# Optimization experiments

Measured on AMD Instinct MI355X. Metric: run time of the kernel, lower is better.

## Reference

```python
import jax, jax.numpy as jnp
import numpy as np

B, LN, LT, D, DIN, H = 8, 64, 256, 1024, 2048, 4
LN_EPS = 1e-5
F16_EPS = float(np.finfo(np.float16).eps)


def setup_inputs() -> dict:
    key = jax.random.key(0)
    ks = jax.random.split(key, 16)
    n = lambda k, sh: jax.random.normal(k, sh, dtype=jnp.float32)
    s = 0.02
    z = lambda sh: jnp.zeros(sh, jnp.float32)
    return {
        "text_embeds": n(ks[0], (B, LT, D)),
        "node_embeds": n(ks[1], (B, LN, D)),
        "Wq": n(ks[2], (D, H * D)) * s, "bq": z((H * D,)),
        "Wk": n(ks[3], (D, H * D)) * s, "bk": z((H * D,)),
        "Wv": n(ks[4], (D, H * D)) * s, "bv": z((H * D,)),
        "Wo": n(ks[5], (H * D, D)) * s, "bo": z((D,)),
        "ln_g": jnp.ones((D,), jnp.float32), "ln_b": z((D,)),
        "aqW": n(ks[6], (D, D)) * s, "aqb": z((D,)),
        "akW": n(ks[7], (D, D)) * s, "akb": z((D,)),
        "att_v": n(ks[8], (D,)) * (1.0 / np.sqrt(D)),
        "att_b": z((D,)),
        "dp1W": n(ks[9], (D, DIN // 2)) * s, "dp1b": z((DIN // 2,)),
        "dp2W": n(ks[10], (DIN // 2, DIN)) * s, "dp2b": z((DIN,)),
        "gnn_mask": jax.random.randint(ks[11], (B, LN), 0, 2),
        "lm_mask": jax.random.randint(ks[12], (B, LT), 0, 2),
    }


def _forward(text_embeds, node_embeds, Wq, bq, Wk, bk, Wv, bv, Wo, bo, ln_g, ln_b,
             aqW, aqb, akW, akb, att_v, att_b, dp1W, dp1b, dp2W, dp2b,
             gnn_mask, lm_mask):
    x = node_embeds  # (B, LN, D)

    # ---- selfAttention_prompt: each of 4 heads has full width D ----
    def heads(w, b):
        return (x @ w + b).reshape(B, LN, H, D).transpose(0, 2, 1, 3)  # (B,H,LN,D)

    Q, K, V = heads(Wq, bq), heads(Wk, bk), heads(Wv, bv)
    A = jnp.einsum('bhqd,bhkd->bhqk', Q, K) / jnp.sqrt(jnp.float32(D))
    A = jnp.where(gnn_mask[:, None, None, :] == 0, -jnp.inf, A)
    alpha = jax.nn.softmax(A, axis=-1)
    out = jnp.einsum('bhqk,bhkd->bhqd', alpha, V)
    out = out.transpose(0, 2, 1, 3).reshape(B, LN, H * D)
    out = out @ Wo + bo + x
    # LayerNorm (torch default eps=1e-5)
    mu = out.mean(-1, keepdims=True)
    var = ((out - mu) ** 2).mean(-1, keepdims=True)
    H2 = (out - mu) / jnp.sqrt(var + LN_EPS) * ln_g + ln_b  # (B, LN, D)

    # ---- AdditiveAttention (Bahdanau): value_proj is unused in the original ----
    q = H2 @ aqW + aqb            # (B, LN, D)
    k = text_embeds @ akW + akb   # (B, LT, D)
    e = jnp.einsum('bqkd,d->bqk',
                   jnp.tanh(q[:, :, None, :] + k[:, None, :, :] + att_b), att_v)
    e = jnp.where(lm_mask[:, None, :] == 0, -jnp.inf, e)
    w = jax.nn.softmax(e, axis=-1)            # (B, LN, LT)
    H3 = jnp.einsum('bqk,bkd->bqd', w, text_embeds)  # context with raw V

    # ---- filter_Pool: masked mean over nodes ----
    m = gnn_mask.astype(H3.dtype)[:, :, None]
    cnt = jnp.clip(m.sum(1), F16_EPS, None)   # (B, 1)
    H4 = (H3 * m).sum(1) / cnt                # (B, D)

    # ---- domain projector (exact GELU like torch) ----
    Z = jax.nn.gelu(H4 @ dp1W + dp1b, approximate=False) @ dp2W + dp2b
    return Z  # (B, DIN)


def reference(text_embeds, node_embeds, Wq, bq, Wk, bk, Wv, bv, Wo, bo, ln_g, ln_b,
              aqW, aqb, akW, akb, att_v, att_b, dp1W, dp1b, dp2W, dp2b,
              gnn_mask, lm_mask):
    return _forward(text_embeds, node_embeds, Wq, bq, Wk, bk, Wv, bv, Wo, bo,
                    ln_g, ln_b, aqW, aqb, akW, akb, att_v, att_b,
                    dp1W, dp1b, dp2W, dp2b, gnn_mask, lm_mask)
```

## Files before the change

### kernel.cpp

```cpp
#include <hip/hip_runtime.h>
#include <hip/hip_bf16.h>
#include <math.h>

#define NB 8
#define LNN 64
#define LTN 256
#define DD 1024
#define NH 4
#define HDD 4096
#define DINN 2048
#define DHN 1024

#define C_TANH 2.8853900817779268f

typedef __bf16 bf16x8 __attribute__((ext_vector_type(8)));
typedef float f32x4 __attribute__((ext_vector_type(4)));

__device__ __forceinline__ ushort f2b(float f) {
  unsigned int u = __builtin_bit_cast(unsigned int, f);
  u = (u + 0x7FFFu + ((u >> 16) & 1u)) >> 16;
  return (ushort)u;
}

__global__ __launch_bounds__(256) void prep(const float* __restrict__ node,
                                            ushort* __restrict__ node_bf,
                                            const float* __restrict__ text,
                                            ushort* __restrict__ text_bf,
                                            const float* __restrict__ Wq,
                                            const float* __restrict__ Wk,
                                            const float* __restrict__ Wv,
                                            const float* __restrict__ Wo,
                                            const float* __restrict__ aqW,
                                            const float* __restrict__ akW,
                                            ushort* __restrict__ TwtQKV,
                                            ushort* __restrict__ TwtWo,
                                            ushort* __restrict__ TwtAQ) {
  int bid = blockIdx.x;
  int t = threadIdx.x;
  if (bid < 1280) {
    const float* in;
    ushort* out;
    int i;
    if (bid < 256) { in = node; out = node_bf; i = (bid * 256 + t) * 8; }
    else { in = text; out = text_bf; i = ((bid - 256) * 256 + t) * 8; }
    float4 a = *(const float4*)(in + i);
    float4 b = *(const float4*)(in + i + 4);
    ushort4 o0 = {f2b(a.x), f2b(a.y), f2b(a.z), f2b(a.w)};
    ushort4 o1 = {f2b(b.x), f2b(b.y), f2b(b.z), f2b(b.w)};
    *(ushort4*)(out + i) = o0;
    *(ushort4*)(out + i + 4) = o1;
    return;
  }
  bid -= 1280;
  const float* W;
  ushort* dst0;
  int K, N, tt;
  if (bid < 3072) {
    int z = bid >> 10;
    tt = bid & 1023;
    W = (z == 0) ? Wq : ((z == 1) ? Wk : Wv);
    dst0 = TwtQKV + (size_t)z * DD * HDD;
    K = DD; N = HDD;
  } else if (bid < 4096) {
    tt = bid - 3072; W = Wo; dst0 = TwtWo; K = HDD; N = DD;
  } else if (bid < 4352) {
    tt = bid - 4096; W = aqW; dst0 = TwtAQ; K = DD; N = DD;
  } else {
    tt = bid - 4352; W = akW; dst0 = TwtAQ + (size_t)DD * DD; K = DD; N = DD;
  }
  int ntn = N >> 6;
  int n0 = (tt % ntn) << 6, k0 = (tt / ntn) << 6;
  __shared__ float tf[64][65];
  int r = t >> 2, c4 = (t & 3) * 16;
  const float* src = W + (size_t)(k0 + r) * N + n0 + c4;
  float4 v0 = *(const float4*)(src);
  float4 v1 = *(const float4*)(src + 4);
  float4 v2 = *(const float4*)(src + 8);
  float4 v3 = *(const float4*)(src + 12);
  *(float4*)&tf[r][c4] = v0;
  *(float4*)&tf[r][c4 + 4] = v1;
  *(float4*)&tf[r][c4 + 8] = v2;
  *(float4*)&tf[r][c4 + 12] = v3;
  __syncthreads();
  int nl = t >> 2, kc = (t & 3) * 16;
  ushort tmp[16];
#pragma unroll
  for (int j = 0; j < 16; ++j) tmp[j] = f2b(tf[kc + j][nl]);
  ushort* dst = dst0 + (size_t)(n0 + nl) * K + k0 + kc;
  *(uint4*)(dst) = *(uint4*)&tmp[0];
  *(uint4*)(dst + 8) = *(uint4*)&tmp[8];
}

__global__ __launch_bounds__(256) void gemm_qkv3(const ushort* __restrict__ A,
                                                 const ushort* __restrict__ BtB,
                                                 const float* __restrict__ b0,
                                                 const float* __restrict__ b1,
                                                 const float* __restrict__ b2,
                                                 ushort* __restrict__ o0,
                                                 ushort* __restrict__ o1,
                                                 ushort* __restrict__ o2,
                                                 int M, int N, int K) {
  int z = blockIdx.z;
  const ushort* Bt = BtB + (size_t)z * N * K;
  const float* bias = (z == 0) ? b0 : ((z == 1) ? b1 : b2);
  ushort* Cout = (z == 0) ? o0 : ((z == 1) ? o1 : o2);
  __shared__ ushort Als[64 * 64];
  __shared__ ushort Bls[128 * 64];
  int tid = threadIdx.x;
  int m0 = blockIdx.y << 6, n0 = blockIdx.x << 7;
  int srow = tid >> 3, su = tid & 7;
  int sx = (su ^ (srow & 7)) * 8;
  const ushort* ga = A + (size_t)(m0 + srow) * K + su * 8;
  const ushort* gb = Bt + (size_t)(n0 + srow) * K + su * 8;
  int wa0 = srow * 64 + sx, wa1 = (srow + 32) * 64 + sx;
  int wb2 = (srow + 64) * 64 + sx, wb3 = (srow + 96) * 64 + sx;
  const size_t rs32 = (size_t)32 * K;
  int lane = tid & 63, w = tid >> 6;
  int wm = w >> 1, wn = w & 1;
  int r = lane & 15, kg = lane >> 4;
  f32x4 acc[2][4] = {};
  uint4 pa0 = *(const uint4*)(ga);
  uint4 pa1 = *(const uint4*)(ga + rs32);
  uint4 pb0 = *(const uint4*)(gb);
  uint4 pb1 = *(const uint4*)(gb + rs32);
  uint4 pb2 = *(const uint4*)(gb + 2 * rs32);
  uint4 pb3 = *(const uint4*)(gb + 3 * rs32);
  for (int k0 = 0; k0 < K; k0 += 64) {
    __syncthreads();
    *(uint4*)&Als[wa0] = pa0; *(uint4*)&Als[wa1] = pa1;
    *(uint4*)&Bls[wa0] = pb0; *(uint4*)&Bls[wa1] = pb1;
    *(uint4*)&Bls[wb2] = pb2; *(uint4*)&Bls[wb3] = pb3;
    __syncthreads();
    int kn = k0 + 64;
    if (kn < K) {
      pa0 = *(const uint4*)(ga + kn);
      pa1 = *(const uint4*)(ga + rs32 + kn);
      pb0 = *(const uint4*)(gb + kn);
      pb1 = *(const uint4*)(gb + rs32 + kn);
      pb2 = *(const uint4*)(gb + 2 * rs32 + kn);
      pb3 = *(const uint4*)(gb + 3 * rs32 + kn);
    }
#pragma unroll
    for (int h = 0; h < 2; ++h) {
      int sa = ((h * 4 + kg) ^ (r & 7)) * 8;
      bf16x8 af[2], bfr[4];
#pragma unroll
      for (int m = 0; m < 2; ++m)
        af[m] = *(const bf16x8*)&Als[(wm * 32 + m * 16 + r) * 64 + sa];
#pragma unroll
      for (int n = 0; n < 4; ++n)
        bfr[n] = *(const bf16x8*)&Bls[(wn * 64 + n * 16 + r) * 64 + sa];
#pragma unroll
      for (int m = 0; m < 2; ++m)
#pragma unroll
        for (int n = 0; n < 4; ++n)
          acc[m][n] = __builtin_amdgcn_mfma_f32_16x16x32_bf16(af[m], bfr[n], acc[m][n], 0, 0, 0);
    }
  }
#pragma unroll
  for (int m = 0; m < 2; ++m)
#pragma unroll
    for (int n = 0; n < 4; ++n) {
      f32x4 a = acc[m][n];
#pragma unroll
      for (int v = 0; v < 4; ++v) {
        int row = m0 + wm * 32 + m * 16 + kg * 4 + v;
        int col = n0 + wn * 64 + n * 16 + r;
        Cout[(size_t)row * N + col] = f2b(a[v] + bias[col]);
      }
    }
}

__global__ __launch_bounds__(256) void gemm_wo_split(const ushort* __restrict__ A,
                                                     const ushort* __restrict__ Bt,
                                                     float* __restrict__ P,
                                                     int M, int N, int K) {
  __shared__ ushort Als[64 * 64];
  __shared__ ushort Bls[128 * 64];
  int tid = threadIdx.x;
  int m0 = blockIdx.y << 6, n0 = blockIdx.x << 7;
  int Ks = K >> 2, kbase = blockIdx.z * Ks;
  int srow = tid >> 3, su = tid & 7;
  int sx = (su ^ (srow & 7)) * 8;
  const ushort* ga = A + (size_t)(m0 + srow) * K + kbase + su * 8;
  const ushort* gb = Bt + (size_t)(n0 + srow) * K + kbase + su * 8;
  int wa0 = srow * 64 + sx, wa1 = (srow + 32) * 64 + sx;
  int wb2 = (srow + 64) * 64 + sx, wb3 = (srow + 96) * 64 + sx;
  const size_t rs32 = (size_t)32 * K;
  int lane = tid & 63, w = tid >> 6;
  int wm = w >> 1, wn = w & 1;
  int r = lane & 15, kg = lane >> 4;
  f32x4 acc[2][4] = {};
  uint4 pa0 = *(const uint4*)(ga);
  uint4 pa1 = *(const uint4*)(ga + rs32);
  uint4 pb0 = *(const uint4*)(gb);
  uint4 pb1 = *(const uint4*)(gb + rs32);
  uint4 pb2 = *(const uint4*)(gb + 2 * rs32);
  uint4 pb3 = *(const uint4*)(gb + 3 * rs32);
  for (int k0 = 0; k0 < Ks; k0 += 64) {
    __syncthreads();
    *(uint4*)&Als[wa0] = pa0; *(uint4*)&Als[wa1] = pa1;
    *(uint4*)&Bls[wa0] = pb0; *(uint4*)&Bls[wa1] = pb1;
    *(uint4*)&Bls[wb2] = pb2; *(uint4*)&Bls[wb3] = pb3;
    __syncthreads();
    int kn = k0 + 64;
    if (kn < Ks) {
      pa0 = *(const uint4*)(ga + kn);
      pa1 = *(const uint4*)(ga + rs32 + kn);
      pb0 = *(const uint4*)(gb + kn);
      pb1 = *(const uint4*)(gb + rs32 + kn);
      pb2 = *(const uint4*)(gb + 2 * rs32 + kn);
      pb3 = *(const uint4*)(gb + 3 * rs32 + kn);
    }
#pragma unroll
    for (int h = 0; h < 2; ++h) {
      int sa = ((h * 4 + kg) ^ (r & 7)) * 8;
      bf16x8 af[2], bfr[4];
#pragma unroll
      for (int m = 0; m < 2; ++m)
        af[m] = *(const bf16x8*)&Als[(wm * 32 + m * 16 + r) * 64 + sa];
#pragma unroll
      for (int n = 0; n < 4; ++n)
        bfr[n] = *(const bf16x8*)&Bls[(wn * 64 + n * 16 + r) * 64 + sa];
#pragma unroll
      for (int m = 0; m < 2; ++m)
#pragma unroll
        for (int n = 0; n < 4; ++n)
          acc[m][n] = __builtin_amdgcn_mfma_f32_16x16x32_bf16(af[m], bfr[n], acc[m][n], 0, 0, 0);
    }
  }
#pragma unroll
  for (int m = 0; m < 2; ++m)
#pragma unroll
    for (int n = 0; n < 4; ++n) {
      f32x4 a = acc[m][n];
#pragma unroll
      for (int v = 0; v < 4; ++v) {
        int row = m0 + wm * 32 + m * 16 + kg * 4 + v;
        int col = n0 + wn * 64 + n * 16 + r;
        P[((size_t)blockIdx.z * M + row) * N + col] = a[v];
      }
    }
}

__global__ __launch_bounds__(256) void gemm_aqak(const ushort* __restrict__ H2,
                                                 const ushort* __restrict__ Tbf,
                                                 const ushort* __restrict__ TwtAQ,
                                                 const float* __restrict__ aqb,
                                                 const float* __restrict__ akb,
                                                 const float* __restrict__ attb,
                                                 float* __restrict__ QBu,
                                                 float* __restrict__ KAB,
                                                 int N, int K) {
  __shared__ ushort Als[64 * 64];
  __shared__ ushort Bls[128 * 64];
  int tid = threadIdx.x;
  int gm0 = blockIdx.y << 6, n0 = blockIdx.x << 7;
  const ushort* Abase;
  const ushort* Bt;
  const float* bias;
  const float* bias2;
  float* Obase;
  if (gm0 < 512) {
    Abase = H2 + (size_t)gm0 * K;
    Bt = TwtAQ;
    bias = aqb; bias2 = nullptr;
    Obase = QBu + (size_t)gm0 * N;
  } else {
    Abase = Tbf + (size_t)(gm0 - 512) * K;
    Bt = TwtAQ + (size_t)N * K;
    bias = akb; bias2 = attb;
    Obase = KAB + (size_t)(gm0 - 512) * N;
  }
  int srow = tid >> 3, su = tid & 7;
  int sx = (su ^ (srow & 7)) * 8;
  const ushort* ga = Abase + (size_t)srow * K + su * 8;
  const ushort* gb = Bt + (size_t)(n0 + srow) * K + su * 8;
  int wa0 = srow * 64 + sx, wa1 = (srow + 32) * 64 + sx;
  int wb2 = (srow + 64) * 64 + sx, wb3 = (srow + 96) * 64 + sx;
  const size_t rs32 = (size_t)32 * K;
  int lane = tid & 63, w = tid >> 6;
  int wm = w >> 1, wn = w & 1;
  int r = lane & 15, kg = lane >> 4;
  f32x4 acc[2][4] = {};
  uint4 pa0 = *(const uint4*)(ga);
  uint4 pa1 = *(const uint4*)(ga + rs32);
  uint4 pb0 = *(const uint4*)(gb);
  uint4 pb1 = *(const uint4*)(gb + rs32);
  uint4 pb2 = *(const uint4*)(gb + 2 * rs32);
  uint4 pb3 = *(const uint4*)(gb + 3 * rs32);
  for (int k0 = 0; k0 < K; k0 += 64) {
    __syncthreads();
    *(uint4*)&Als[wa0] = pa0; *(uint4*)&Als[wa1] = pa1;
    *(uint4*)&Bls[wa0] = pb0; *(uint4*)&Bls[wa1] = pb1;
    *(uint4*)&Bls[wb2] = pb2; *(uint4*)&Bls[wb3] = pb3;
    __syncthreads();
    int kn = k0 + 64;
    if (kn < K) {
      pa0 = *(const uint4*)(ga + kn);
      pa1 = *(const uint4*)(ga + rs32 + kn);
      pb0 = *(const uint4*)(gb + kn);
      pb1 = *(const uint4*)(gb + rs32 + kn);
      pb2 = *(const uint4*)(gb + 2 * rs32 + kn);
      pb3 = *(const uint4*)(gb + 3 * rs32 + kn);
    }
#pragma unroll
    for (int h = 0; h < 2; ++h) {
      int sa = ((h * 4 + kg) ^ (r & 7)) * 8;
      bf16x8 af[2], bfr[4];
#pragma unroll
      for (int m = 0; m < 2; ++m)
        af[m] = *(const bf16x8*)&Als[(wm * 32 + m * 16 + r) * 64 + sa];
#pragma unroll
      for (int n = 0; n < 4; ++n)
        bfr[n] = *(const bf16x8*)&Bls[(wn * 64 + n * 16 + r) * 64 + sa];
#pragma unroll
      for (int m = 0; m < 2; ++m)
#pragma unroll
        for (int n = 0; n < 4; ++n)
          acc[m][n] = __builtin_amdgcn_mfma_f32_16x16x32_bf16(af[m], bfr[n], acc[m][n], 0, 0, 0);
    }
  }
#pragma unroll
  for (int m = 0; m < 2; ++m)
#pragma unroll
    for (int n = 0; n < 4; ++n) {
      f32x4 a = acc[m][n];
#pragma unroll
      for (int v = 0; v < 4; ++v) {
        int lrow = wm * 32 + m * 16 + kg * 4 + v;
        int col = n0 + wn * 64 + n * 16 + r;
        float x = a[v] + bias[col];
        if (bias2) x += bias2[col];
        Obase[(size_t)lrow * N + col] = x * C_TANH;
      }
    }
}

__global__ __launch_bounds__(256) void wo_ln(const float* __restrict__ P,
                                             const float* __restrict__ bo,
                                             const float* __restrict__ node,
                                             const float* __restrict__ g,
                                             const float* __restrict__ be,
                                             ushort* __restrict__ Y) {
  int row = blockIdx.x, tid = threadIdx.x;
  int c = tid * 4;
  const size_t MN = (size_t)512 * 1024;
  size_t o = (size_t)row * DD + c;
  float4 v0 = *(const float4*)(P + o);
  float4 v1 = *(const float4*)(P + MN + o);
  float4 v2 = *(const float4*)(P + 2 * MN + o);
  float4 v3 = *(const float4*)(P + 3 * MN + o);
  float4 rv = *(const float4*)(node + o);
  float4 bv = *(const float4*)(bo + c);
  float4 v;
  v.x = v0.x + v1.x + v2.x + v3.x + rv.x + bv.x;
  v.y = v0.y + v1.y + v2.y + v3.y + rv.y + bv.y;
  v.z = v0.z + v1.z + v2.z + v3.z + rv.z + bv.z;
  v.w = v0.w + v1.w + v2.w + v3.w + rv.w + bv.w;
  float s = v.x + v.y + v.z + v.w;
  float ss = v.x * v.x + v.y * v.y + v.z * v.z + v.w * v.w;
  for (int o2 = 32; o2; o2 >>= 1) {
    s += __shfl_xor(s, o2, 64);
    ss += __shfl_xor(ss, o2, 64);
  }
  __shared__ float rb_[8];
  int lane = tid & 63, w = tid >> 6;
  if (lane == 0) { rb_[w] = s; rb_[4 + w] = ss; }
  __syncthreads();
  s = rb_[0] + rb_[1] + rb_[2] + rb_[3];
  ss = rb_[4] + rb_[5] + rb_[6] + rb_[7];
  float mu = s * (1.f / 1024.f);
  float var = ss * (1.f / 1024.f) - mu * mu;
  float rstd = rsqrtf(var + 1e-5f);
  ushort4 o4;
  o4.x = f2b((v.x - mu) * rstd * g[c + 0] + be[c + 0]);
  o4.y = f2b((v.y - mu) * rstd * g[c + 1] + be[c + 1]);
  o4.z = f2b((v.z - mu) * rstd * g[c + 2] + be[c + 2]);
  o4.w = f2b((v.w - mu) * rstd * g[c + 3] + be[c + 3]);
  *(ushort4*)(Y + (size_t)row * DD + c) = o4;
}

__global__ __launch_bounds__(256) void attn_one(const ushort* __restrict__ Qb,
                                                const ushort* __restrict__ Kb,
                                                const ushort* __restrict__ Vb,
                                                const int* __restrict__ gmask,
                                                ushort* __restrict__ AO) {
  int bid = blockIdx.x;
  int bh = bid >> 3, dt = bid & 7;
  int b = bh >> 2;
  int d0 = dt * 128;
  size_t base = ((size_t)b * LNN) * HDD + (size_t)(bh & 3) * DD;
  __shared__ ushort Als[64 * 64];
  __shared__ ushort Bls[64 * 64];
  __shared__ float S[64][68];
  __shared__ ushort Pls[64 * 72];
  __shared__ ushort Vt[128 * 72];
  int tid = threadIdx.x;
  int lane = tid & 63, w = tid >> 6;
  int wm = w >> 1, wn = w & 1;
  int r = lane & 15, kg = lane >> 4;
  {
    int srow = tid >> 2, su0 = (tid & 3) * 2;
    const ushort* ga = Qb + base + (size_t)srow * HDD + su0 * 8;
    const ushort* gb = Kb + base + (size_t)srow * HDD + su0 * 8;
    int wa0 = srow * 64 + ((su0) ^ (srow & 7)) * 8;
    int wa1 = srow * 64 + ((su0 + 1) ^ (srow & 7)) * 8;
    f32x4 acc[2][2] = {};
    uint4 pa0 = *(const uint4*)(ga);
    uint4 pa1 = *(const uint4*)(ga + 8);
    uint4 pb0 = *(const uint4*)(gb);
    uint4 pb1 = *(const uint4*)(gb + 8);
    for (int k0 = 0; k0 < DD; k0 += 64) {
      __syncthreads();
      *(uint4*)&Als[wa0] = pa0; *(uint4*)&Als[wa1] = pa1;
      *(uint4*)&Bls[wa0] = pb0; *(uint4*)&Bls[wa1] = pb1;
      __syncthreads();
      int kn = k0 + 64;
      if (kn < DD) {
        pa0 = *(const uint4*)(ga + kn);
        pa1 = *(const uint4*)(ga + kn + 8);
        pb0 = *(const uint4*)(gb + kn);
        pb1 = *(const uint4*)(gb + kn + 8);
      }
#pragma unroll
      for (int h = 0; h < 2; ++h) {
        int sa = ((h * 4 + kg) ^ (r & 7)) * 8;
        bf16x8 af[2], bfr[2];
#pragma unroll
        for (int m = 0; m < 2; ++m)
          af[m] = *(const bf16x8*)&Als[(wm * 32 + m * 16 + r) * 64 + sa];
#pragma unroll
        for (int n = 0; n < 2; ++n)
          bfr[n] = *(const bf16x8*)&Bls[(wn * 32 + n * 16 + r) * 64 + sa];
#pragma unroll
        for (int m = 0; m < 2; ++m)
#pragma unroll
          for (int n = 0; n < 2; ++n)
            acc[m][n] = __builtin_amdgcn_mfma_f32_16x16x32_bf16(af[m], bfr[n], acc[m][n], 0, 0, 0);
      }
    }
#pragma unroll
    for (int m = 0; m < 2; ++m)
#pragma unroll
      for (int n = 0; n < 2; ++n)
#pragma unroll
        for (int v = 0; v < 4; ++v)
          S[wm * 32 + m * 16 + kg * 4 + v][wn * 32 + n * 16 + r] = acc[m][n][v];
  }
  {
    int kq = lane, dq = w * 32;
    const ushort* src = Vb + base + (size_t)kq * HDD + d0 + dq;
    uint4 v0 = *(const uint4*)src;
    uint4 v1 = *(const uint4*)(src + 8);
    uint4 v2 = *(const uint4*)(src + 16);
    uint4 v3 = *(const uint4*)(src + 24);
    ushort tmp[32];
    *(uint4*)&tmp[0] = v0; *(uint4*)&tmp[8] = v1;
    *(uint4*)&tmp[16] = v2; *(uint4*)&tmp[24] = v3;
#pragma unroll
    for (int j = 0; j < 32; ++j) Vt[(dq + j) * 72 + kq] = tmp[j];
  }
  __syncthreads();
  bool valid = gmask[b * LNN + lane] != 0;
  for (int i = 0; i < 16; ++i) {
    int q = w * 16 + i;
    float v = valid ? S[q][lane] * 0.03125f : -__builtin_inff();
    float mx = v;
    for (int o = 32; o; o >>= 1) mx = fmaxf(mx, __shfl_xor(mx, o, 64));
    float e = valid ? __expf(v - mx) : 0.f;
    float s = e;
    for (int o = 32; o; o >>= 1) s += __shfl_xor(s, o, 64);
    Pls[q * 72 + lane] = f2b(__fdividef(e, s));
  }
  __syncthreads();
  f32x4 acc[2][4] = {};
#pragma unroll
  for (int h = 0; h < 2; ++h) {
    int ko = h * 32 + kg * 8;
    bf16x8 af[2], bfr[4];
#pragma unroll
    for (int m = 0; m < 2; ++m)
      af[m] = *(const bf16x8*)&Pls[(wm * 32 + m * 16 + r) * 72 + ko];
#pragma unroll
    for (int n = 0; n < 4; ++n)
      bfr[n] = *(const bf16x8*)&Vt[(wn * 64 + n * 16 + r) * 72 + ko];
#pragma unroll
    for (int m = 0; m < 2; ++m)
#pragma unroll
      for (int n = 0; n < 4; ++n)
        acc[m][n] = __builtin_amdgcn_mfma_f32_16x16x32_bf16(af[m], bfr[n], acc[m][n], 0, 0, 0);
  }
#pragma unroll
  for (int m = 0; m < 2; ++m)
#pragma unroll
    for (int n = 0; n < 4; ++n) {
      f32x4 a = acc[m][n];
#pragma unroll
      for (int v = 0; v < 4; ++v) {
        int q = wm * 32 + m * 16 + kg * 4 + v;
        int col = wn * 64 + n * 16 + r;
        AO[base + (size_t)q * HDD + d0 + col] = f2b(a[v]);
      }
    }
}

__global__ __launch_bounds__(256) void addatt_e(const float* __restrict__ QBu,
                                                const float* __restrict__ KAB,
                                                const float* __restrict__ av_,
                                                float* __restrict__ E8) {
  int ds = blockIdx.x, qt = blockIdx.y, b = blockIdx.z;
  int tid = threadIdx.x;
  __shared__ float qs[8][128];
  __shared__ float avs[128];
  __shared__ float red[4];
  int bq0 = b * LNN + qt * 8;
  {
    int qq = tid >> 5, dd = (tid & 31) * 4;
    *(float4*)&qs[qq][dd] = *(const float4*)(QBu + (size_t)(bq0 + qq) * DD + ds * 128 + dd);
  }
  float av = (tid < 128) ? av_[ds * 128 + tid] : 0.f;
  if (tid < 128) avs[tid] = av;
  float s = av;
  for (int o = 32; o; o >>= 1) s += __shfl_xor(s, o, 64);
  int lane = tid & 63, w = tid >> 6;
  if (lane == 0) red[w] = s;
  __syncthreads();
  float sumav = red[0] + red[1] + red[2] + red[3];
  const float* kr = KAB + (size_t)(b * LTN + tid) * DD + ds * 128;
  float ac[8] = {};
#pragma unroll 2
  for (int d = 0; d < 128; d += 4) {
    float4 kv = *(const float4*)(kr + d);
    float4 av4 = *(const float4*)&avs[d];
#pragma unroll
    for (int qq = 0; qq < 8; ++qq) {
      float4 q4 = *(const float4*)&qs[qq][d];
      ac[qq] = fmaf(av4.x, __builtin_amdgcn_rcpf(__builtin_amdgcn_exp2f(q4.x + kv.x) + 1.f), ac[qq]);
      ac[qq] = fmaf(av4.y, __builtin_amdgcn_rcpf(__builtin_amdgcn_exp2f(q4.y + kv.y) + 1.f), ac[qq]);
      ac[qq] = fmaf(av4.z, __builtin_amdgcn_rcpf(__builtin_amdgcn_exp2f(q4.z + kv.z) + 1.f), ac[qq]);
      ac[qq] = fmaf(av4.w, __builtin_amdgcn_rcpf(__builtin_amdgcn_exp2f(q4.w + kv.w) + 1.f), ac[qq]);
    }
  }
  size_t ebase = ((size_t)ds * 512 + bq0) * LTN + tid;
#pragma unroll
  for (int qq = 0; qq < 8; ++qq)
    E8[ebase + (size_t)qq * LTN] = sumav - 2.f * ac[qq];
}

__global__ __launch_bounds__(256) void addatt_sm(const float* __restrict__ E8,
                                                 const int* __restrict__ lmask,
                                                 float* __restrict__ Wv) {
  int bq = blockIdx.x;
  int b = bq >> 6;
  int tid = threadIdx.x;
  __shared__ float rb_[8];
  float e = 0.f;
#pragma unroll
  for (int ks = 0; ks < 8; ++ks)
    e += E8[((size_t)ks * 512 + bq) * LTN + tid];
  bool valid = lmask[b * LTN + tid] != 0;
  float v = valid ? e : -__builtin_inff();
  int lane = tid & 63, w = tid >> 6;
  float m = v;
  for (int o = 32; o; o >>= 1) m = fmaxf(m, __shfl_xor(m, o, 64));
  if (lane == 0) rb_[w] = m;
  __syncthreads();
  m = fmaxf(fmaxf(rb_[0], rb_[1]), fmaxf(rb_[2], rb_[3]));
  float ex = valid ? __expf(v - m) : 0.f;
  float sm = ex;
  for (int o = 32; o; o >>= 1) sm += __shfl_xor(sm, o, 64);
  if (lane == 0) rb_[4 + w] = sm;
  __syncthreads();
  sm = rb_[4] + rb_[5] + rb_[6] + rb_[7];
  Wv[(size_t)bq * LTN + tid] = __fdividef(ex, sm);
}

__global__ __launch_bounds__(256) void addatt_pool(const float* __restrict__ Wv,
                                                   const float* __restrict__ text,
                                                   const int* __restrict__ gmask,
                                                   float* __restrict__ H4) {
  int dt = blockIdx.x, b = blockIdx.y;
  int tid = threadIdx.x;
  __shared__ float cf[LTN];
  float c = 0.f, cnt = 0.f;
#pragma unroll 8
  for (int q = 0; q < LNN; ++q) {
    float m = (gmask[b * LNN + q] != 0) ? 1.f : 0.f;
    cnt += m;
    c = fmaf(m, Wv[(size_t)(b * LNN + q) * LTN + tid], c);
  }
  cf[tid] = c;
  cnt = fmaxf(cnt, 9.765625e-04f);
  __syncthreads();
  int d = dt * 256 + tid;
  const float* tb = text + (size_t)b * LTN * DD + d;
  float acc = 0.f;
#pragma unroll 8
  for (int k = 0; k < LTN; ++k) acc = fmaf(cf[k], tb[(size_t)k * DD], acc);
  H4[b * DD + d] = acc / cnt;
}

__global__ __launch_bounds__(256) void dp_split(const float* __restrict__ X,
                                                const float* __restrict__ W,
                                                float* __restrict__ P,
                                                int K, int N) {
  int jt = blockIdx.x, kt = blockIdx.y;
  int t = threadIdx.x;
  __shared__ float xs[8][32];
  if (t < 64) {
    int b = t >> 3, kk = (t & 7) * 4;
    *(float4*)&xs[b][kk] = *(const float4*)(X + (size_t)b * K + kt * 32 + kk);
  }
  __syncthreads();
  int j = jt * 64 + (t & 63);
  int bg = (t >> 6) * 2;
  const float* wp = W + (size_t)(kt * 32) * N + j;
  float a0 = 0.f, a1 = 0.f;
#pragma unroll
  for (int k = 0; k < 32; ++k) {
    float w = wp[(size_t)k * N];
    a0 = fmaf(xs[bg + 0][k], w, a0);
    a1 = fmaf(xs[bg + 1][k], w, a1);
  }
  P[((size_t)kt * 8 + bg + 0) * N + j] = a0;
  P[((size_t)kt * 8 + bg + 1) * N + j] = a1;
}

__global__ __launch_bounds__(256) void dp_split2g(const float* __restrict__ P1,
                                                  const float* __restrict__ b1,
                                                  const float* __restrict__ W,
                                                  float* __restrict__ P,
                                                  int K, int N) {
  int jt = blockIdx.x, kt = blockIdx.y;
  int t = threadIdx.x;
  __shared__ float xs[8][32];
  {
    int b = t >> 5, kk = t & 31;
    int j = kt * 32 + kk;
    float s = b1[j];
#pragma unroll 8
    for (int p = 0; p < 32; ++p) s += P1[((size_t)p * 8 + b) * K + j];
    xs[b][kk] = 0.5f * s * (1.f + erff(s * 0.70710678118654752440f));
  }
  __syncthreads();
  int j = jt * 64 + (t & 63);
  int bg = (t >> 6) * 2;
  const float* wp = W + (size_t)(kt * 32) * N + j;
  float a0 = 0.f, a1 = 0.f;
#pragma unroll
  for (int k = 0; k < 32; ++k) {
    float w = wp[(size_t)k * N];
    a0 = fmaf(xs[bg + 0][k], w, a0);
    a1 = fmaf(xs[bg + 1][k], w, a1);
  }
  P[((size_t)kt * 8 + bg + 0) * N + j] = a0;
  P[((size_t)kt * 8 + bg + 1) * N + j] = a1;
}

template <int GELU>
__global__ __launch_bounds__(256) void dp_reduce(const float* __restrict__ P,
                                                 const float* __restrict__ bias,
                                                 float* __restrict__ O, int N) {
  int b = blockIdx.y;
  int j = blockIdx.x * 256 + threadIdx.x;
  float s = bias[j];
#pragma unroll 8
  for (int kt = 0; kt < 32; ++kt) s += P[((size_t)kt * 8 + b) * N + j];
  if constexpr (GELU) s = 0.5f * s * (1.f + erff(s * 0.70710678118654752440f));
  O[(size_t)b * N + j] = s;
}

extern "C" void kernel_launch(void* const* d_in, const int* in_sizes, int n_in,
                              void* d_out, int out_size, void* d_ws, size_t ws_size,
                              hipStream_t stream) {
  const float* text = (const float*)d_in[0];
  const float* node = (const float*)d_in[1];
  const float* Wq = (const float*)d_in[2];
  const float* bq = (const float*)d_in[3];
  const float* Wk = (const float*)d_in[4];
  const float* bk = (const float*)d_in[5];
  const float* Wv = (const float*)d_in[6];
  const float* bv = (const float*)d_in[7];
  const float* Wo = (const float*)d_in[8];
  const float* bo = (const float*)d_in[9];
  const float* lng = (const float*)d_in[10];
  const float* lnb = (const float*)d_in[11];
  const float* aqW = (const float*)d_in[12];
  const float* aqb = (const float*)d_in[13];
  const float* akW = (const float*)d_in[14];
  const float* akb = (const float*)d_in[15];
  const float* attv = (const float*)d_in[16];
  const float* attb = (const float*)d_in[17];
  const float* dp1W = (const float*)d_in[18];
  const float* dp1b = (const float*)d_in[19];
  const float* dp2W = (const float*)d_in[20];
  const float* dp2b = (const float*)d_in[21];
  const int* gmask = (const int*)d_in[22];
  const int* lmask = (const int*)d_in[23];
  (void)in_sizes; (void)n_in; (void)out_size; (void)ws_size;

  char* base = (char*)d_ws;
#define MB(x) (((size_t)(x)) << 20)
  ushort* TwtQKV = (ushort*)(base);
  ushort* TwtWo = (ushort*)(base + MB(24));
  ushort* TwtAQ = (ushort*)(base + MB(32));
  ushort* node_bf = (ushort*)(base + MB(36));
  ushort* text_bf = (ushort*)(base + MB(37));
  ushort* Qb = (ushort*)(base + MB(41));
  ushort* Kb = (ushort*)(base + MB(45));
  ushort* Vb = (ushort*)(base + MB(49));
  ushort* AO = (ushort*)(base + MB(53));
  float* P_Wo = (float*)(base + MB(61));
  ushort* H2 = (ushort*)(base + MB(69));
  float* QBu = (float*)(base + MB(70));
  float* KAB = (float*)(base + MB(72));
  float* E8 = (float*)(base + MB(80));
  float* Wvb = (float*)(base + MB(84));
  float* H4 = (float*)(base + MB(84) + (512 << 10));
  float* P1 = (float*)(base + MB(85));
  float* P2 = (float*)(base + MB(86));
  float* Z = (float*)d_out;
#undef MB

  const int M1 = NB * LNN;
  dim3 blk(256);

  prep<<<dim3(5888), blk, 0, stream>>>(node, node_bf, text, text_bf,
                                       Wq, Wk, Wv, Wo, aqW, akW,
                                       TwtQKV, TwtWo, TwtAQ);

  gemm_qkv3<<<dim3(HDD / 128, M1 / 64, 3), blk, 0, stream>>>(node_bf, TwtQKV, bq, bk, bv, Qb, Kb, Vb, M1, HDD, DD);

  attn_one<<<dim3(NB * NH * 8), blk, 0, stream>>>(Qb, Kb, Vb, gmask, AO);

  gemm_wo_split<<<dim3(DD / 128, M1 / 64, 4), blk, 0, stream>>>(AO, TwtWo, P_Wo, M1, DD, HDD);
  wo_ln<<<dim3(M1), blk, 0, stream>>>(P_Wo, bo, node, lng, lnb, H2);

  gemm_aqak<<<dim3(DD / 128, 40), blk, 0, stream>>>(H2, text_bf, TwtAQ, aqb, akb, attb, QBu, KAB, DD, DD);

  addatt_e<<<dim3(8, 8, NB), blk, 0, stream>>>(QBu, KAB, attv, E8);
  addatt_sm<<<dim3(M1), blk, 0, stream>>>(E8, lmask, Wvb);
  addatt_pool<<<dim3(4, NB), blk, 0, stream>>>(Wvb, text, gmask, H4);

  dp_split<<<dim3(DHN / 64, 32), blk, 0, stream>>>(H4, dp1W, P1, DD, DHN);
  dp_split2g<<<dim3(DINN / 64, 32), blk, 0, stream>>>(P1, dp1b, dp2W, P2, DHN, DINN);
  dp_reduce<0><<<dim3(DINN / 256, NB), blk, 0, stream>>>(P2, dp2b, Z, DINN);
}
```

Measured before the change: 160.8 us.

## Merge text key projection GEMM into the Wo split-K GEMM launch

```diff
diff --git a/kernel.cpp b/kernel.cpp
--- a/kernel.cpp
+++ b/kernel.cpp
@@ -171,18 +171,38 @@
     }
 }
 
-__global__ __launch_bounds__(256) void gemm_wo_split(const ushort* __restrict__ A,
-                                                     const ushort* __restrict__ Bt,
-                                                     float* __restrict__ P,
-                                                     int M, int N, int K) {
+__global__ __launch_bounds__(256) void gemm_wo_ak(const ushort* __restrict__ AO,
+                                                  const ushort* __restrict__ TwtWo,
+                                                  const ushort* __restrict__ Tbf,
+                                                  const ushort* __restrict__ TwtAK,
+                                                  const float* __restrict__ akb,
+                                                  const float* __restrict__ attb,
+                                                  float* __restrict__ P_Wo,
+                                                  float* __restrict__ KAB) {
+  int bid = blockIdx.x;
+  bool isWo = bid < 256;
+  const ushort* Abase;
+  const ushort* Bt;
+  int m0, n0, K, Ks, kbase, N;
+  if (isWo) {
+    n0 = (bid & 7) << 7;
+    m0 = ((bid >> 3) & 7) << 6;
+    int ks = bid >> 6;
+    K = HDD; Ks = HDD >> 2; kbase = ks * Ks;
+    Abase = AO; Bt = TwtWo; N = DD;
+  } else {
+    int b2 = bid - 256;
+    n0 = (b2 & 7) << 7;
+    m0 = (b2 >> 3) << 6;
+    K = DD; Ks = DD; kbase = 0;
+    Abase = Tbf; Bt = TwtAK; N = DD;
+  }
   __shared__ ushort Als[64 * 64];
   __shared__ ushort Bls[128 * 64];
   int tid = threadIdx.x;
-  int m0 = blockIdx.y << 6, n0 = blockIdx.x << 7;
-  int Ks = K >> 2, kbase = blockIdx.z * Ks;
   int srow = tid >> 3, su = tid & 7;
   int sx = (su ^ (srow & 7)) * 8;
-  const ushort* ga = A + (size_t)(m0 + srow) * K + kbase + su * 8;
+  const ushort* ga = Abase + (size_t)(m0 + srow) * K + kbase + su * 8;
   const ushort* gb = Bt + (size_t)(n0 + srow) * K + kbase + su * 8;
   int wa0 = srow * 64 + sx, wa1 = (srow + 32) * 64 + sx;
   int wb2 = (srow + 64) * 64 + sx, wb3 = (srow + 96) * 64 + sx;
@@ -229,53 +249,49 @@
           acc[m][n] = __builtin_amdgcn_mfma_f32_16x16x32_bf16(af[m], bfr[n], acc[m][n], 0, 0, 0);
     }
   }
-#pragma unroll
-  for (int m = 0; m < 2; ++m)
-#pragma unroll
-    for (int n = 0; n < 4; ++n) {
-      f32x4 a = acc[m][n];
-#pragma unroll
-      for (int v = 0; v < 4; ++v) {
-        int row = m0 + wm * 32 + m * 16 + kg * 4 + v;
-        int col = n0 + wn * 64 + n * 16 + r;
-        P[((size_t)blockIdx.z * M + row) * N + col] = a[v];
+  if (isWo) {
+    int ks = bid >> 6;
+#pragma unroll
+    for (int m = 0; m < 2; ++m)
+#pragma unroll
+      for (int n = 0; n < 4; ++n) {
+        f32x4 a = acc[m][n];
+#pragma unroll
+        for (int v = 0; v < 4; ++v) {
+          int row = m0 + wm * 32 + m * 16 + kg * 4 + v;
+          int col = n0 + wn * 64 + n * 16 + r;
+          P_Wo[((size_t)ks * 512 + row) * DD + col] = a[v];
+        }
       }
-    }
-}
-
-__global__ __launch_bounds__(256) void gemm_aqak(const ushort* __restrict__ H2,
-                                                 const ushort* __restrict__ Tbf,
-                                                 const ushort* __restrict__ TwtAQ,
-                                                 const float* __restrict__ aqb,
-                                                 const float* __restrict__ akb,
-                                                 const float* __restrict__ attb,
-                                                 float* __restrict__ QBu,
-                                                 float* __restrict__ KAB,
-                                                 int N, int K) {
+  } else {
+#pragma unroll
+    for (int m = 0; m < 2; ++m)
+#pragma unroll
+      for (int n = 0; n < 4; ++n) {
+        f32x4 a = acc[m][n];
+#pragma unroll
+        for (int v = 0; v < 4; ++v) {
+          int row = m0 + wm * 32 + m * 16 + kg * 4 + v;
+          int col = n0 + wn * 64 + n * 16 + r;
+          KAB[(size_t)row * DD + col] = (a[v] + akb[col] + attb[col]) * C_TANH;
+        }
+      }
+  }
+}
+
+__global__ __launch_bounds__(256) void gemm_aq(const ushort* __restrict__ H2,
+                                               const ushort* __restrict__ TwtAQ,
+                                               const float* __restrict__ aqb,
+                                               float* __restrict__ QBu,
+                                               int M, int N, int K) {
   __shared__ ushort Als[64 * 64];
   __shared__ ushort Bls[128 * 64];
   int tid = threadIdx.x;
-  int gm0 = blockIdx.y << 6, n0 = blockIdx.x << 7;
-  const ushort* Abase;
-  const ushort* Bt;
-  const float* bias;
-  const float* bias2;
-  float* Obase;
-  if (gm0 < 512) {
-    Abase = H2 + (size_t)gm0 * K;
-    Bt = TwtAQ;
-    bias = aqb; bias2 = nullptr;
-    Obase = QBu + (size_t)gm0 * N;
-  } else {
-    Abase = Tbf + (size_t)(gm0 - 512) * K;
-    Bt = TwtAQ + (size_t)N * K;
-    bias = akb; bias2 = attb;
-    Obase = KAB + (size_t)(gm0 - 512) * N;
-  }
+  int m0 = blockIdx.y << 6, n0 = blockIdx.x << 7;
   int srow = tid >> 3, su = tid & 7;
   int sx = (su ^ (srow & 7)) * 8;
-  const ushort* ga = Abase + (size_t)srow * K + su * 8;
-  const ushort* gb = Bt + (size_t)(n0 + srow) * K + su * 8;
+  const ushort* ga = H2 + (size_t)(m0 + srow) * K + su * 8;
+  const ushort* gb = TwtAQ + (size_t)(n0 + srow) * K + su * 8;
   int wa0 = srow * 64 + sx, wa1 = (srow + 32) * 64 + sx;
   int wb2 = (srow + 64) * 64 + sx, wb3 = (srow + 96) * 64 + sx;
   const size_t rs32 = (size_t)32 * K;
@@ -328,11 +344,9 @@
       f32x4 a = acc[m][n];
 #pragma unroll
       for (int v = 0; v < 4; ++v) {
-        int lrow = wm * 32 + m * 16 + kg * 4 + v;
+        int row = m0 + wm * 32 + m * 16 + kg * 4 + v;
         int col = n0 + wn * 64 + n * 16 + r;
-        float x = a[v] + bias[col];
-        if (bias2) x += bias2[col];
-        Obase[(size_t)lrow * N + col] = x * C_TANH;
+        QBu[(size_t)row * N + col] = (a[v] + aqb[col]) * C_TANH;
       }
     }
 }
@@ -734,10 +748,11 @@
 
   attn_one<<<dim3(NB * NH * 8), blk, 0, stream>>>(Qb, Kb, Vb, gmask, AO);
 
-  gemm_wo_split<<<dim3(DD / 128, M1 / 64, 4), blk, 0, stream>>>(AO, TwtWo, P_Wo, M1, DD, HDD);
+  gemm_wo_ak<<<dim3(512), blk, 0, stream>>>(AO, TwtWo, text_bf, TwtAQ + (size_t)DD * DD,
+                                            akb, attb, P_Wo, KAB);
   wo_ln<<<dim3(M1), blk, 0, stream>>>(P_Wo, bo, node, lng, lnb, H2);
 
-  gemm_aqak<<<dim3(DD / 128, 40), blk, 0, stream>>>(H2, text_bf, TwtAQ, aqb, akb, attb, QBu, KAB, DD, DD);
+  gemm_aq<<<dim3(DD / 128, M1 / 64), blk, 0, stream>>>(H2, TwtAQ, aqb, QBu, M1, DD, DD);
 
   addatt_e<<<dim3(8, 8, NB), blk, 0, stream>>>(QBu, KAB, attv, E8);
   addatt_sm<<<dim3(M1), blk, 0, stream>>>(E8, lmask, Wvb);
```

Result: no change. 159.2 us (-1.0%).
